# Kernel optimization log

Measured on AMD Instinct MI355X. Metric: run time of the kernel, lower is better.

The kernel has to match this reference:

```python
import jax, jax.numpy as jnp
import numpy as np

TOPK, NC, ALPHA, BETA, EPS = 13, 80, 1.0, 6.0, 1e-9


def make_anchors():
    # YOLOv8 anchor centers for a 640x640 image, strides 8/16/32 -> 8400 points
    pts = []
    for s in (8, 16, 32):
        n = 640 // s
        yv, xv = jnp.meshgrid(jnp.arange(n, dtype=jnp.float32) + 0.5,
                              jnp.arange(n, dtype=jnp.float32) + 0.5, indexing='ij')
        pts.append(jnp.stack([xv, yv], -1).reshape(-1, 2) * s)
    return jnp.concatenate(pts, 0)  # (8400, 2)


def setup_inputs() -> dict:
    key = jax.random.key(0)
    ks = jax.random.split(key, 5)
    B, NMAX = 32, 64
    anc_points = make_anchors()
    A = anc_points.shape[0]
    pd_scores = jax.random.uniform(ks[0], (B, A, NC), jnp.float32)
    # predicted boxes: anchor-centered xyxy with random extents
    half = jax.random.uniform(ks[1], (B, A, 2), jnp.float32) * 32.0 + 2.0
    ctr = anc_points[None]
    pd_bboxes = jnp.concatenate([ctr - half, ctr + half], -1)
    # gt boxes: valid xyxy inside the 640x640 image
    xy = jax.random.uniform(ks[2], (B, NMAX, 2), jnp.float32) * 520.0
    wh = jax.random.uniform(ks[3], (B, NMAX, 2), jnp.float32) * 120.0 + 8.0
    gt_bboxes = jnp.concatenate([xy, xy + wh], -1)
    gt_labels = jax.random.randint(ks[4], (B, NMAX, 1), 0, NC).astype(jnp.int64)
    mask_gt = jnp.ones((B, NMAX, 1), jnp.float32)
    return {"pd_scores": pd_scores, "pd_bboxes": pd_bboxes, "anc_points": anc_points,
            "gt_labels": gt_labels, "gt_bboxes": gt_bboxes, "mask_gt": mask_gt}


def _iou_xyxy(box1, box2, eps=1e-7):
    # box1: (B, N, 1, 4), box2: (B, 1, A, 4) -> iou (B, N, A)
    lt = jnp.maximum(box1[..., :2], box2[..., :2])
    rb = jnp.minimum(box1[..., 2:], box2[..., 2:])
    wh = jnp.clip(rb - lt, 0.0)
    inter = wh[..., 0] * wh[..., 1]
    a1 = (box1[..., 2] - box1[..., 0]) * (box1[..., 3] - box1[..., 1])
    a2 = (box2[..., 2] - box2[..., 0]) * (box2[..., 3] - box2[..., 1])
    return inter / (a1 + a2 - inter + eps)


def reference(pd_scores, pd_bboxes, anc_points, gt_labels, gt_bboxes, mask_gt):
    B, A, _ = pd_scores.shape
    N = gt_bboxes.shape[1]
    # --- select_candidates_in_gts: anchor center strictly inside gt box ---
    deltas = jnp.concatenate([
        anc_points[None, None] - gt_bboxes[:, :, None, :2],
        gt_bboxes[:, :, None, 2:] - anc_points[None, None]], -1)  # (B,N,A,4)
    mask_in_gts = (deltas.min(-1) > EPS).astype(jnp.float32)       # (B,N,A)
    mask_valid = mask_in_gts * mask_gt                             # mask_gt (B,N,1)
    # --- get_box_metrics ---
    # bbox_scores[b,n,a] = pd_scores[b, a, gt_labels[b,n]]
    bbox_scores = jnp.take_along_axis(pd_scores.transpose(0, 2, 1),
                                      gt_labels, axis=1)           # (B,N,A)
    overlaps = jnp.clip(_iou_xyxy(gt_bboxes[:, :, None], pd_bboxes[:, None]), 0.0)
    align_metric = (bbox_scores ** ALPHA) * (overlaps ** BETA)
    align_metric = align_metric * mask_valid
    overlaps = overlaps * mask_valid
    # --- select_topk_candidates ---
    _, topk_idxs = jax.lax.top_k(align_metric, TOPK)               # (B,N,TOPK)
    bi = jnp.arange(B)[:, None, None]
    ni = jnp.arange(N)[None, :, None]
    mask_topk = jnp.zeros_like(align_metric).at[bi, ni, topk_idxs].set(1.0)
    mask_pos = mask_valid * mask_topk                              # (B,N,A)
    fg_mask = mask_pos.sum(1)                                      # (B,A)
    # multi-GT conflict resolution (always applied; no-op when no conflicts)
    max_metric = align_metric.max(1, keepdims=True)
    mask_pos = jnp.where(fg_mask[:, None, :] > 1,
                         mask_pos * (align_metric == max_metric).astype(mask_pos.dtype),
                         mask_pos)
    fg_mask = mask_pos.sum(1)
    target_gt_idx = jnp.argmax(mask_pos, 1)                        # (B,A)
    # --- targets ---
    b2 = jnp.arange(B)[:, None]
    target_labels = gt_labels[..., 0][b2, target_gt_idx]           # (B,A)
    target_bboxes = gt_bboxes[b2, target_gt_idx]                   # (B,A,4)
    pos_align = (align_metric * mask_pos).max(1)                   # (B,A)
    target_scores = jax.nn.one_hot(target_labels, NC, dtype=jnp.float32) \
        * pos_align[..., None]                                     # (B,A,NC)
    return (target_bboxes, target_scores, fg_mask.astype(bool))
```

## Files before the change

### kernel.cpp

```cpp
#include <hip/hip_runtime.h>

#define BB 32
#define AA 8400
#define NGT 64
#define NCLS 80
#define TOPK 13
#define SLOTS 4

__device__ __forceinline__ void anchor_xy(int a, float& px, float& py) {
    if (a < 6400)      { int y = a / 80;          int x = a - 80 * y;  px = (x + 0.5f) * 8.0f;  py = (y + 0.5f) * 8.0f; }
    else if (a < 8000) { int r = a - 6400; int y = r / 40; int x = r - 40 * y; px = (x + 0.5f) * 16.0f; py = (y + 0.5f) * 16.0f; }
    else               { int r = a - 8000; int y = r / 20; int x = r - 20 * y; px = (x + 0.5f) * 32.0f; py = (y + 0.5f) * 32.0f; }
}

__device__ __forceinline__ float compute_metric(
    const float* __restrict__ pd_scores,
    const float4* __restrict__ pd_bboxes,
    float4 g, int label, int b, int a)
{
    float px, py;
    anchor_xy(a, px, py);
    float dmin = fminf(fminf(px - g.x, py - g.y), fminf(g.z - px, g.w - py));
    if (!(dmin > 1e-9f)) return 0.0f;
    float4 pb = pd_bboxes[b * AA + a];
    float ltx = fmaxf(g.x, pb.x), lty = fmaxf(g.y, pb.y);
    float rbx = fminf(g.z, pb.z), rby = fminf(g.w, pb.w);
    float w = fmaxf(rbx - ltx, 0.0f), h = fmaxf(rby - lty, 0.0f);
    float inter = w * h;
    float a1 = (g.z - g.x) * (g.w - g.y);
    float a2 = (pb.z - pb.x) * (pb.w - pb.y);
    float iou = fmaxf(inter / (a1 + a2 - inter + 1e-7f), 0.0f);
    float s = pd_scores[(size_t)(b * AA + a) * NCLS + label];
    float i2 = iou * iou;
    return s * (i2 * i2 * i2);
}

__global__ __launch_bounds__(256) void k_zero(float4* __restrict__ p, int n4) {
    int i = blockIdx.x * 256 + threadIdx.x;
    if (i < n4) p[i] = make_float4(0.f, 0.f, 0.f, 0.f);
}

__global__ __launch_bounds__(256) void k_topk(
    const float* __restrict__ pd_scores,
    const float4* __restrict__ pd_bboxes,
    const int* __restrict__ gt_labels,
    const float4* __restrict__ gt_bboxes,
    const float* __restrict__ mask_gt,
    unsigned long long* __restrict__ bits)
{
    __shared__ unsigned long long keys[4 * TOPK];
    int gid = blockIdx.x;
    if (mask_gt[gid] <= 0.0f) return;
    int b = gid >> 6, n = gid & 63;
    float4 g = gt_bboxes[gid];
    int label = gt_labels[gid];
    float ga1 = (g.z - g.x) * (g.w - g.y);
    int tid = threadIdx.x;
    int w = tid >> 6, lane = tid & 63;

    if (tid < 4 * TOPK) keys[tid] = 0;

    float va[SLOTS]; int ai[SLOTS]; int cnt = 0;
    #pragma unroll
    for (int j = 0; j < SLOTS; ++j) { va[j] = -1.0f; ai[j] = -1; }

#define SCAN_LEVEL(S, N, OFF)                                                   \
    {                                                                           \
        const float inv = 1.0f / (float)(S);                                    \
        int xlo = (int)floorf(g.x * inv - 0.5f); if (xlo < 0) xlo = 0;          \
        int xhi = (int)ceilf (g.z * inv - 0.5f); if (xhi > (N)-1) xhi = (N)-1;  \
        int ylo = (int)floorf(g.y * inv - 0.5f); if (ylo < 0) ylo = 0;          \
        int yhi = (int)ceilf (g.w * inv - 0.5f); if (yhi > (N)-1) yhi = (N)-1;  \
        int nx = xhi - xlo + 1, ny = yhi - ylo + 1;                             \
        int tot = (nx > 0 && ny > 0) ? nx * ny : 0;                             \
        for (int c = tid; c < tot; c += 256) {                                  \
            int yy = c / nx, xx = c - yy * nx;                                  \
            int gx = xlo + xx, gy = ylo + yy;                                   \
            int a = (OFF) + gy * (N) + gx;                                      \
            float px = (gx + 0.5f) * (float)(S), py = (gy + 0.5f) * (float)(S); \
            float dmin = fminf(fminf(px - g.x, py - g.y),                       \
                               fminf(g.z - px, g.w - py));                      \
            if (dmin > 1e-9f) {                                                 \
                float4 pb = pd_bboxes[b * AA + a];                              \
                float ltx = fmaxf(g.x, pb.x), lty = fmaxf(g.y, pb.y);           \
                float rbx = fminf(g.z, pb.z), rby = fminf(g.w, pb.w);           \
                float wd = fmaxf(rbx - ltx, 0.0f), hg = fmaxf(rby - lty, 0.0f); \
                float inter = wd * hg;                                          \
                float a2 = (pb.z - pb.x) * (pb.w - pb.y);                       \
                float iou = fmaxf(inter / (ga1 + a2 - inter + 1e-7f), 0.0f);    \
                float sc = pd_scores[(size_t)(b * AA + a) * NCLS + label];      \
                float i2 = iou * iou;                                           \
                float v = sc * (i2 * i2 * i2);                                  \
                if (v > 0.0f) {                                                 \
                    _Pragma("unroll")                                           \
                    for (int j = 0; j < SLOTS; ++j)                             \
                        if (j == cnt) { va[j] = v; ai[j] = a; }                 \
                    cnt++;                                                      \
                }                                                               \
            }                                                                   \
        }                                                                       \
    }

    SCAN_LEVEL(8, 80, 0)
    SCAN_LEVEL(16, 40, 6400)
    SCAN_LEVEL(32, 20, 8000)
#undef SCAN_LEVEL

    __syncthreads();

    for (int k = 0; k < TOPK; ++k) {
        unsigned long long key = 0;
        #pragma unroll
        for (int j = 0; j < SLOTS; ++j)
            if (va[j] > 0.0f) {
                unsigned long long kk =
                    ((unsigned long long)__float_as_uint(va[j]) << 32)
                    | (unsigned)(0x7FFFFFFF - ai[j]);
                key = kk > key ? kk : key;
            }
        #pragma unroll
        for (int off = 32; off; off >>= 1) {
            unsigned long long o = __shfl_xor(key, off);
            key = o > key ? o : key;
        }
        if (key == 0) break;
        if (lane == 0) keys[w * TOPK + k] = key;
        int wa = 0x7FFFFFFF - (int)(unsigned)(key & 0xFFFFFFFFull);
        #pragma unroll
        for (int j = 0; j < SLOTS; ++j) if (ai[j] == wa) va[j] = -1.0f;
    }

    __syncthreads();

    if (w == 0) {
        unsigned long long mykey = (lane < 4 * TOPK) ? keys[lane] : 0;
        unsigned long long* mybits = bits + (size_t)b * AA;
        unsigned long long nbit = 1ull << n;
        for (int k = 0; k < TOPK; ++k) {
            unsigned long long best = mykey;
            #pragma unroll
            for (int off = 32; off; off >>= 1) {
                unsigned long long o = __shfl_xor(best, off);
                best = o > best ? o : best;
            }
            if (best == 0) break;
            if (lane == 0) {
                int wa = 0x7FFFFFFF - (int)(unsigned)(best & 0xFFFFFFFFull);
                atomicOr(&mybits[wa], nbit);
            }
            if (mykey == best) mykey = 0;
        }
    }
}

__global__ __launch_bounds__(256) void k_out(
    const float* __restrict__ pd_scores,
    const float4* __restrict__ pd_bboxes,
    const int* __restrict__ gt_labels,
    const float4* __restrict__ gt_bboxes,
    const float* __restrict__ mask_gt,
    const unsigned long long* __restrict__ bits,
    float4* __restrict__ out_bbox,
    float* __restrict__ out_fg,
    float4* __restrict__ out_scores)
{
    __shared__ float s_pos[256];
    __shared__ int   s_lab[256];
    int base = blockIdx.x * 256;
    int idx = base + threadIdx.x;
    int b = idx / AA, a = idx - b * AA;
    unsigned long long m = bits[idx];
    float pos = 0.0f; int tgt = 0; int fg = 0;
    if (m) {
        if (__popcll(m) == 1) {
            int n = __ffsll((unsigned long long)m) - 1;
            float4 g = gt_bboxes[b * NGT + n];
            pos = compute_metric(pd_scores, pd_bboxes, g, gt_labels[b * NGT + n], b, a);
            tgt = n; fg = 1;
        } else {
            float px, py; anchor_xy(a, px, py);
            float4 pb = pd_bboxes[idx];
            float a2 = (pb.z - pb.x) * (pb.w - pb.y);
            float mmax = 0.0f; unsigned long long nb = 0;
            for (int n = 0; n < NGT; ++n) {
                if (mask_gt[b * NGT + n] <= 0.0f) continue;
                float4 g = gt_bboxes[b * NGT + n];
                float dmin = fminf(fminf(px - g.x, py - g.y), fminf(g.z - px, g.w - py));
                if (!(dmin > 1e-9f)) continue;
                float ltx = fmaxf(g.x, pb.x), lty = fmaxf(g.y, pb.y);
                float rbx = fminf(g.z, pb.z), rby = fminf(g.w, pb.w);
                float wd = fmaxf(rbx - ltx, 0.0f), hg = fmaxf(rby - lty, 0.0f);
                float inter = wd * hg;
                float a1 = (g.z - g.x) * (g.w - g.y);
                float iou = fmaxf(inter / (a1 + a2 - inter + 1e-7f), 0.0f);
                float sc = pd_scores[(size_t)idx * NCLS + gt_labels[b * NGT + n]];
                float i2 = iou * iou;
                float v = sc * (i2 * i2 * i2);
                if (v > mmax) { mmax = v; nb = m & (1ull << n); }
                else if (v == mmax && v > 0.0f) nb |= m & (1ull << n);
            }
            if (nb) { tgt = __ffsll(nb) - 1; pos = mmax; fg = 1; }
        }
    }
    out_bbox[idx] = gt_bboxes[b * NGT + tgt];
    out_fg[idx] = fg ? 1.0f : 0.0f;
    s_pos[threadIdx.x] = pos;
    s_lab[threadIdx.x] = gt_labels[b * NGT + tgt];
    __syncthreads();

    float4* dst = out_scores + (size_t)base * (NCLS / 4);
    for (int ci = threadIdx.x; ci < 256 * (NCLS / 4); ci += 256) {
        int an = ci / (NCLS / 4);
        int c0 = (ci - an * (NCLS / 4)) * 4;
        float p = s_pos[an];
        int lb = s_lab[an];
        float4 r = make_float4(0.f, 0.f, 0.f, 0.f);
        if (p != 0.0f) {
            if (lb == c0)     r.x = p;
            if (lb == c0 + 1) r.y = p;
            if (lb == c0 + 2) r.z = p;
            if (lb == c0 + 3) r.w = p;
        }
        dst[ci] = r;
    }
}

extern "C" void kernel_launch(void* const* d_in, const int* in_sizes, int n_in,
                              void* d_out, int out_size, void* d_ws, size_t ws_size,
                              hipStream_t stream) {
    const float*  pd_scores = (const float*) d_in[0];
    const float4* pd_bboxes = (const float4*)d_in[1];
    const int*    gt_labels = (const int*)   d_in[3];
    const float4* gt_bboxes = (const float4*)d_in[4];
    const float*  mask_gt   = (const float*) d_in[5];

    float* out = (float*)d_out;
    float4* out_bbox   = (float4*)out;
    float4* out_scores = (float4*)(out + (size_t)BB * AA * 4);
    float*  out_fg     = out + (size_t)BB * AA * 4 + (size_t)BB * AA * NCLS;

    unsigned long long* bits = (unsigned long long*)d_ws;

    int n4 = BB * AA * 8 / 16;
    k_zero<<<(n4 + 255) / 256, 256, 0, stream>>>((float4*)bits, n4);

    k_topk<<<BB * NGT, 256, 0, stream>>>(pd_scores, pd_bboxes,
                                         gt_labels, gt_bboxes, mask_gt, bits);

    k_out<<<BB * AA / 256, 256, 0, stream>>>(
        pd_scores, pd_bboxes, gt_labels, gt_bboxes, mask_gt, bits,
        out_bbox, out_fg, out_scores);
}
```

Measured before the change: 67.23 us.

## Replace global per-anchor bitmask with compact top-k lists rebuilt in shared memory

The topk kernel now writes a compact list of up to 16 selected anchor indices per GT instead of atomically OR-ing bits into a global per-anchor 64-bit mask. The output kernel processes per-batch chunks of 256 anchors, scans that batch's lists to rebuild the bitmask in shared memory, and caches GT boxes, labels and masks in LDS. This removes the zeroing kernel and the global atomics. In exchange, every output block re-reads the batch's 1024-entry list. The multi-GT path is also unrolled in groups of 8 with branch-free predication.

```diff
diff --git a/kernel.cpp b/kernel.cpp
--- a/kernel.cpp
+++ b/kernel.cpp
@@ -6,38 +6,13 @@
 #define NCLS 80
 #define TOPK 13
 #define SLOTS 4
+#define CHUNK 256
+#define NCHUNK 33
 
 __device__ __forceinline__ void anchor_xy(int a, float& px, float& py) {
     if (a < 6400)      { int y = a / 80;          int x = a - 80 * y;  px = (x + 0.5f) * 8.0f;  py = (y + 0.5f) * 8.0f; }
     else if (a < 8000) { int r = a - 6400; int y = r / 40; int x = r - 40 * y; px = (x + 0.5f) * 16.0f; py = (y + 0.5f) * 16.0f; }
     else               { int r = a - 8000; int y = r / 20; int x = r - 20 * y; px = (x + 0.5f) * 32.0f; py = (y + 0.5f) * 32.0f; }
-}
-
-__device__ __forceinline__ float compute_metric(
-    const float* __restrict__ pd_scores,
-    const float4* __restrict__ pd_bboxes,
-    float4 g, int label, int b, int a)
-{
-    float px, py;
-    anchor_xy(a, px, py);
-    float dmin = fminf(fminf(px - g.x, py - g.y), fminf(g.z - px, g.w - py));
-    if (!(dmin > 1e-9f)) return 0.0f;
-    float4 pb = pd_bboxes[b * AA + a];
-    float ltx = fmaxf(g.x, pb.x), lty = fmaxf(g.y, pb.y);
-    float rbx = fminf(g.z, pb.z), rby = fminf(g.w, pb.w);
-    float w = fmaxf(rbx - ltx, 0.0f), h = fmaxf(rby - lty, 0.0f);
-    float inter = w * h;
-    float a1 = (g.z - g.x) * (g.w - g.y);
-    float a2 = (pb.z - pb.x) * (pb.w - pb.y);
-    float iou = fmaxf(inter / (a1 + a2 - inter + 1e-7f), 0.0f);
-    float s = pd_scores[(size_t)(b * AA + a) * NCLS + label];
-    float i2 = iou * iou;
-    return s * (i2 * i2 * i2);
-}
-
-__global__ __launch_bounds__(256) void k_zero(float4* __restrict__ p, int n4) {
-    int i = blockIdx.x * 256 + threadIdx.x;
-    if (i < n4) p[i] = make_float4(0.f, 0.f, 0.f, 0.f);
 }
 
 __global__ __launch_bounds__(256) void k_topk(
@@ -46,17 +21,20 @@
     const int* __restrict__ gt_labels,
     const float4* __restrict__ gt_bboxes,
     const float* __restrict__ mask_gt,
-    unsigned long long* __restrict__ bits)
+    int* __restrict__ list)
 {
     __shared__ unsigned long long keys[4 * TOPK];
     int gid = blockIdx.x;
-    if (mask_gt[gid] <= 0.0f) return;
-    int b = gid >> 6, n = gid & 63;
+    int tid = threadIdx.x;
+    int w = tid >> 6, lane = tid & 63;
+    if (mask_gt[gid] <= 0.0f) {
+        if (tid < 16) list[gid * 16 + tid] = -1;
+        return;
+    }
+    int b = gid >> 6;
     float4 g = gt_bboxes[gid];
     int label = gt_labels[gid];
     float ga1 = (g.z - g.x) * (g.w - g.y);
-    int tid = threadIdx.x;
-    int w = tid >> 6, lane = tid & 63;
 
     if (tid < 4 * TOPK) keys[tid] = 0;
 
@@ -134,8 +112,7 @@
 
     if (w == 0) {
         unsigned long long mykey = (lane < 4 * TOPK) ? keys[lane] : 0;
-        unsigned long long* mybits = bits + (size_t)b * AA;
-        unsigned long long nbit = 1ull << n;
+        int kc = 0;
         for (int k = 0; k < TOPK; ++k) {
             unsigned long long best = mykey;
             #pragma unroll
@@ -144,12 +121,13 @@
                 best = o > best ? o : best;
             }
             if (best == 0) break;
-            if (lane == 0) {
-                int wa = 0x7FFFFFFF - (int)(unsigned)(best & 0xFFFFFFFFull);
-                atomicOr(&mybits[wa], nbit);
-            }
+            if (lane == 0)
+                list[gid * 16 + k] = 0x7FFFFFFF - (int)(unsigned)(best & 0xFFFFFFFFull);
+            kc++;
             if (mykey == best) mykey = 0;
         }
+        if (lane == 0)
+            for (int k = kc; k < 16; ++k) list[gid * 16 + k] = -1;
     }
 }
 
@@ -159,61 +137,114 @@
     const int* __restrict__ gt_labels,
     const float4* __restrict__ gt_bboxes,
     const float* __restrict__ mask_gt,
-    const unsigned long long* __restrict__ bits,
+    const int* __restrict__ list,
     float4* __restrict__ out_bbox,
     float* __restrict__ out_fg,
     float4* __restrict__ out_scores)
 {
-    __shared__ float s_pos[256];
-    __shared__ int   s_lab[256];
-    int base = blockIdx.x * 256;
-    int idx = base + threadIdx.x;
-    int b = idx / AA, a = idx - b * AA;
-    unsigned long long m = bits[idx];
-    float pos = 0.0f; int tgt = 0; int fg = 0;
-    if (m) {
-        if (__popcll(m) == 1) {
-            int n = __ffsll((unsigned long long)m) - 1;
-            float4 g = gt_bboxes[b * NGT + n];
-            pos = compute_metric(pd_scores, pd_bboxes, g, gt_labels[b * NGT + n], b, a);
-            tgt = n; fg = 1;
-        } else {
+    __shared__ unsigned int s_lo[CHUNK], s_hi[CHUNK];
+    __shared__ float4 s_gt[NGT];
+    __shared__ int    s_glab[NGT];
+    __shared__ float  s_gmsk[NGT];
+    __shared__ float  s_pos[CHUNK];
+    __shared__ int    s_alab[CHUNK];
+
+    int bidx = blockIdx.x;
+    int b = bidx / NCHUNK;
+    int chunk = bidx - b * NCHUNK;
+    int abase = chunk * CHUNK;
+    int count = AA - abase; if (count > CHUNK) count = CHUNK;
+    int tid = threadIdx.x;
+
+    s_lo[tid] = 0; s_hi[tid] = 0;
+    if (tid < NGT) {
+        s_gt[tid]   = gt_bboxes[b * NGT + tid];
+        s_glab[tid] = gt_labels[b * NGT + tid];
+        s_gmsk[tid] = mask_gt[b * NGT + tid];
+    }
+    __syncthreads();
+
+    const int* blist = list + b * NGT * 16;
+    #pragma unroll
+    for (int e = tid; e < NGT * 16; e += 256) {
+        int a = blist[e];
+        int rel = a - abase;
+        if (a >= 0 && rel >= 0 && rel < count) {
+            int n = e >> 4;
+            if (n < 32) atomicOr(&s_lo[rel], 1u << n);
+            else        atomicOr(&s_hi[rel], 1u << (n - 32));
+        }
+    }
+    __syncthreads();
+
+    if (tid < count) {
+        int a = abase + tid;
+        int idx = b * AA + a;
+        unsigned long long m = ((unsigned long long)s_hi[tid] << 32) | s_lo[tid];
+        float pos = 0.0f; int tgt = 0; int fg = 0;
+        if (m) {
             float px, py; anchor_xy(a, px, py);
             float4 pb = pd_bboxes[idx];
             float a2 = (pb.z - pb.x) * (pb.w - pb.y);
-            float mmax = 0.0f; unsigned long long nb = 0;
-            for (int n = 0; n < NGT; ++n) {
-                if (mask_gt[b * NGT + n] <= 0.0f) continue;
-                float4 g = gt_bboxes[b * NGT + n];
-                float dmin = fminf(fminf(px - g.x, py - g.y), fminf(g.z - px, g.w - py));
-                if (!(dmin > 1e-9f)) continue;
+            if (__popcll(m) == 1) {
+                int n = __ffsll((unsigned long long)m) - 1;
+                float4 g = s_gt[n];
                 float ltx = fmaxf(g.x, pb.x), lty = fmaxf(g.y, pb.y);
                 float rbx = fminf(g.z, pb.z), rby = fminf(g.w, pb.w);
                 float wd = fmaxf(rbx - ltx, 0.0f), hg = fmaxf(rby - lty, 0.0f);
                 float inter = wd * hg;
                 float a1 = (g.z - g.x) * (g.w - g.y);
                 float iou = fmaxf(inter / (a1 + a2 - inter + 1e-7f), 0.0f);
-                float sc = pd_scores[(size_t)idx * NCLS + gt_labels[b * NGT + n]];
+                float sc = pd_scores[(size_t)idx * NCLS + s_glab[n]];
                 float i2 = iou * iou;
-                float v = sc * (i2 * i2 * i2);
-                if (v > mmax) { mmax = v; nb = m & (1ull << n); }
-                else if (v == mmax && v > 0.0f) nb |= m & (1ull << n);
+                pos = sc * (i2 * i2 * i2);
+                tgt = n; fg = 1;
+            } else {
+                float mmax = 0.0f; unsigned long long nb = 0;
+                for (int j0 = 0; j0 < NGT; j0 += 8) {
+                    float v[8];
+                    #pragma unroll
+                    for (int j = 0; j < 8; ++j) {
+                        int n = j0 + j;
+                        float4 g = s_gt[n];
+                        float sc = pd_scores[(size_t)idx * NCLS + s_glab[n]];
+                        float dmin = fminf(fminf(px - g.x, py - g.y),
+                                           fminf(g.z - px, g.w - py));
+                        float ltx = fmaxf(g.x, pb.x), lty = fmaxf(g.y, pb.y);
+                        float rbx = fminf(g.z, pb.z), rby = fminf(g.w, pb.w);
+                        float wd = fmaxf(rbx - ltx, 0.0f), hg = fmaxf(rby - lty, 0.0f);
+                        float inter = wd * hg;
+                        float a1 = (g.z - g.x) * (g.w - g.y);
+                        float iou = fmaxf(inter / (a1 + a2 - inter + 1e-7f), 0.0f);
+                        float i2 = iou * iou;
+                        bool ok = (s_gmsk[n] > 0.0f) && (dmin > 1e-9f);
+                        v[j] = ok ? sc * (i2 * i2 * i2) : 0.0f;
+                    }
+                    #pragma unroll
+                    for (int j = 0; j < 8; ++j) {
+                        int n = j0 + j;
+                        float vv = v[j];
+                        if (vv > mmax) { mmax = vv; nb = m & (1ull << n); }
+                        else if (vv == mmax && vv > 0.0f) nb |= m & (1ull << n);
+                    }
+                }
+                if (nb) { tgt = __ffsll(nb) - 1; pos = mmax; fg = 1; }
             }
-            if (nb) { tgt = __ffsll(nb) - 1; pos = mmax; fg = 1; }
-        }
-    }
-    out_bbox[idx] = gt_bboxes[b * NGT + tgt];
-    out_fg[idx] = fg ? 1.0f : 0.0f;
-    s_pos[threadIdx.x] = pos;
-    s_lab[threadIdx.x] = gt_labels[b * NGT + tgt];
-    __syncthreads();
-
-    float4* dst = out_scores + (size_t)base * (NCLS / 4);
-    for (int ci = threadIdx.x; ci < 256 * (NCLS / 4); ci += 256) {
+        }
+        out_bbox[idx] = s_gt[tgt];
+        out_fg[idx] = fg ? 1.0f : 0.0f;
+        s_pos[tid] = pos;
+        s_alab[tid] = s_glab[tgt];
+    }
+    __syncthreads();
+
+    float4* dst = out_scores + (size_t)(b * AA + abase) * (NCLS / 4);
+    int total = count * (NCLS / 4);
+    for (int ci = tid; ci < total; ci += 256) {
         int an = ci / (NCLS / 4);
         int c0 = (ci - an * (NCLS / 4)) * 4;
         float p = s_pos[an];
-        int lb = s_lab[an];
+        int lb = s_alab[an];
         float4 r = make_float4(0.f, 0.f, 0.f, 0.f);
         if (p != 0.0f) {
             if (lb == c0)     r.x = p;
@@ -239,15 +270,12 @@
     float4* out_scores = (float4*)(out + (size_t)BB * AA * 4);
     float*  out_fg     = out + (size_t)BB * AA * 4 + (size_t)BB * AA * NCLS;
 
-    unsigned long long* bits = (unsigned long long*)d_ws;
-
-    int n4 = BB * AA * 8 / 16;
-    k_zero<<<(n4 + 255) / 256, 256, 0, stream>>>((float4*)bits, n4);
+    int* list = (int*)d_ws;
 
     k_topk<<<BB * NGT, 256, 0, stream>>>(pd_scores, pd_bboxes,
-                                         gt_labels, gt_bboxes, mask_gt, bits);
-
-    k_out<<<BB * AA / 256, 256, 0, stream>>>(
-        pd_scores, pd_bboxes, gt_labels, gt_bboxes, mask_gt, bits,
+                                         gt_labels, gt_bboxes, mask_gt, list);
+
+    k_out<<<BB * NCHUNK, 256, 0, stream>>>(
+        pd_scores, pd_bboxes, gt_labels, gt_bboxes, mask_gt, list,
         out_bbox, out_fg, out_scores);
 }
```

Measured after the change: 67.83 us. Within noise of the previous version (+0.9%).
